# Optimization experiments

Measured on AMD Instinct MI355X. Metric: run time of the kernel, lower is better.

## Reference

```python
import jax, jax.numpy as jnp
import numpy as np

NUM_CLASSES = 80
NUM_ANCHORS = 5
ANCHORS = np.array([[1.3221, 1.73145], [3.19275, 4.00944], [5.05587, 8.09892],
                    [9.47112, 4.84053], [11.2364, 10.0071]], dtype=np.float32)
OBJECT_SCALE = 5.0
NOOBJECT_SCALE = 1.0
COORD_SCALE = 1.0
CLASS_SCALE = 1.0
THRESH = 0.6
SEEN = 0  # module initializes self.seen = 0 -> burn-in branch (seen < 12800) active
MAX_BOXES = 50


def _iou_cxcywh(a, b):
    # a, b: (..., 4) center-x, center-y, w, h; broadcastable. Matches multi_bbox_ious(x1y1x2y2=False).
    ax1, ax2 = a[..., 0] - a[..., 2] / 2, a[..., 0] + a[..., 2] / 2
    ay1, ay2 = a[..., 1] - a[..., 3] / 2, a[..., 1] + a[..., 3] / 2
    bx1, bx2 = b[..., 0] - b[..., 2] / 2, b[..., 0] + b[..., 2] / 2
    by1, by2 = b[..., 1] - b[..., 3] / 2, b[..., 1] + b[..., 3] / 2
    iw = jnp.maximum(jnp.minimum(ax2, bx2) - jnp.maximum(ax1, bx1), 0.0)
    ih = jnp.maximum(jnp.minimum(ay2, by2) - jnp.maximum(ay1, by1), 0.0)
    inter = iw * ih
    union = a[..., 2] * a[..., 3] + b[..., 2] * b[..., 3] - inter
    return inter / jnp.maximum(union, 1e-10)


def setup_inputs() -> dict:
    key = jax.random.key(0)
    k1, k2, k3, k4, k5, k6 = jax.random.split(key, 6)
    nB, nH, nW = 64, 38, 38
    output = jax.random.normal(k1, (nB, NUM_ANCHORS * (5 + NUM_CLASSES), nH, nW), dtype=jnp.float32)
    # target rows: (class, x, y, w, h), coords normalized to (0,1); x>0 keeps all 50 boxes valid
    cls = jax.random.randint(k2, (nB, MAX_BOXES), 0, NUM_CLASSES).astype(jnp.float32)
    x = jax.random.uniform(k3, (nB, MAX_BOXES), minval=0.05, maxval=0.95)
    y = jax.random.uniform(k4, (nB, MAX_BOXES), minval=0.05, maxval=0.95)
    w = jax.random.uniform(k5, (nB, MAX_BOXES), minval=0.02, maxval=0.4)
    h = jax.random.uniform(k6, (nB, MAX_BOXES), minval=0.02, maxval=0.4)
    target = jnp.stack([cls, x, y, w, h], axis=-1).reshape(nB, MAX_BOXES * 5)
    return {"output": output, "target": target}


def _forward(output, target):
    nB, nA, nC = output.shape[0], NUM_ANCHORS, NUM_CLASSES
    nH, nW = output.shape[2], output.shape[3]
    N = nB * nA * nH * nW
    anchors = jnp.asarray(ANCHORS)
    f32 = output.dtype

    out5 = output.reshape(nB, nA, 5 + nC, nH, nW)
    txy = jax.nn.sigmoid(out5[:, :, 0:2])  # [nB,nA,2,nH,nW]
    twh = out5[:, :, 2:4]
    conf = jax.nn.sigmoid(out5[:, :, 4]).reshape(N)
    cls_logits = out5[:, :, 5:].transpose(0, 1, 3, 4, 2).reshape(N, nC)
    # coord layout matches torch: [4, nB*nA*nH*nW], rows = (sx, sy, tw, th)
    coord = jnp.concatenate([txy, twh], axis=2).transpose(2, 0, 1, 3, 4).reshape(4, N)

    # decoded pred boxes in grid units; detached like the original (convert2cpu + .detach())
    grid_x = jnp.arange(nW, dtype=f32)
    grid_y = jnp.arange(nH, dtype=f32)[:, None]
    px = txy[:, :, 0] + grid_x
    py = txy[:, :, 1] + grid_y
    pw = jnp.exp(twh[:, :, 0]) * anchors[:, 0][None, :, None, None]
    ph = jnp.exp(twh[:, :, 1]) * anchors[:, 1][None, :, None, None]
    pred_boxes = jax.lax.stop_gradient(jnp.stack([px, py, pw, ph], axis=-1))  # [nB,nA,nH,nW,4]

    # ---------------- build_targets, vectorized over (batch, gt-box) ----------------
    tbox = target.reshape(nB, MAX_BOXES, 5)  # (cls, x, y, w, h)
    # loop breaks at first x == 0 -> prefix-valid mask
    valid = jnp.cumprod((tbox[:, :, 1] > 0).astype(jnp.int32), axis=1).astype(bool)
    gx, gy = tbox[:, :, 1] * nW, tbox[:, :, 2] * nH
    gw, gh = tbox[:, :, 3] * nW, tbox[:, :, 4] * nH
    gt = jnp.stack([gx, gy, gw, gh], axis=-1)  # [nB,50,4]

    # pass 1: ignore mask -- max IoU of every pred box against all valid GTs
    pb_flat = pred_boxes.reshape(nB, nA * nH * nW, 4)
    ious = _iou_cxcywh(pb_flat[:, :, None, :], gt[:, None, :, :])  # [nB,P,50]
    cur_ious = jnp.where(valid[:, None, :], ious, 0.0).max(axis=2)
    noobj = (cur_ious <= THRESH).astype(f32).reshape(N)

    # pass 2: best anchor per GT (both boxes centered at origin -> IoU simplifies)
    aw, ah = anchors[:, 0], anchors[:, 1]
    inter_a = jnp.minimum(aw, gw[..., None]) * jnp.minimum(ah, gh[..., None])  # [nB,50,nA]
    union_a = aw * ah + (gw * gh)[..., None] - inter_a
    best_n = jnp.argmax(inter_a / jnp.maximum(union_a, 1e-10), axis=-1)  # [nB,50]

    gi = jnp.clip(gx.astype(jnp.int32), 0, nW - 1)
    gj = jnp.clip(gy.astype(jnp.int32), 0, nH - 1)
    b_idx = jnp.arange(nB)[:, None]
    pred_sel = pred_boxes[b_idx, best_n, gj, gi]  # [nB,50,4]
    iou_sel = _iou_cxcywh(gt, pred_sel)           # [nB,50]

    fidx = ((b_idx * nA + best_n) * nH + gj) * nW + gi
    fidx = jnp.where(valid, fidx, N)  # invalid boxes -> OOB index, dropped by scatter

    obj = jnp.zeros(N, f32).at[fidx].set(1.0, mode='drop')
    noobj = noobj.at[fidx].set(0.0, mode='drop')
    cm0 = 0.01 if SEEN < 12800 else 0.0
    coord_mask = jnp.full(N, cm0, f32).at[fidx].set(2.0 - tbox[:, :, 3] * tbox[:, :, 4], mode='drop')
    t0 = 0.5 if SEEN < 12800 else 0.0
    tc0 = jnp.full(N, t0, f32).at[fidx].set(gx - gi.astype(f32), mode='drop')
    tc1 = jnp.full(N, t0, f32).at[fidx].set(gy - gj.astype(f32), mode='drop')
    tc2 = jnp.zeros(N, f32).at[fidx].set(jnp.log(gw / aw[best_n]), mode='drop')
    tc3 = jnp.zeros(N, f32).at[fidx].set(jnp.log(gh / ah[best_n]), mode='drop')
    tcoord = jnp.stack([tc0, tc1, tc2, tc3], axis=0)  # [4,N]
    tconf = jnp.zeros(N, f32).at[fidx].set(iou_sel, mode='drop')  # rescore=1
    tcls = jnp.zeros(N, jnp.int32).at[fidx].set(tbox[:, :, 0].astype(jnp.int32), mode='drop')

    # ---------------- losses ----------------
    conf_mask = OBJECT_SCALE * obj + NOOBJECT_SCALE * noobj
    loss_coord = COORD_SCALE * jnp.sum(((coord - tcoord) * coord_mask) ** 2) / nB
    loss_conf = jnp.sum(((conf - tconf) * conf_mask) ** 2) / nB
    logp = jax.nn.log_softmax(cls_logits, axis=-1)
    ce = -jnp.take_along_axis(logp, tcls[:, None], axis=1)[:, 0]  # per-cell CE
    loss_cls = CLASS_SCALE * jnp.sum(obj * ce) / nB  # CE summed only over obj cells
    return loss_coord + loss_conf + loss_cls


def reference(output, target):
    return _forward(output, target)
```

## Files before the change

kernel.cpp:

```cpp
#include <hip/hip_runtime.h>
#include <math.h>

#define NB 64
#define NA 5
#define NC 80
#define NH 38
#define NW 38
#define MAXB 50
#define PLANE (NH*NW)
#define PER_B (NA*PLANE)
#define NCH (5+NC)
#define MAIN_BX ((PER_B + 255) / 256)
#define NPART (MAIN_BX * NB)

__constant__ float c_aw[5] = {1.3221f, 3.19275f, 5.05587f, 9.47112f, 11.2364f};
__constant__ float c_ah[5] = {1.73145f, 4.00944f, 8.09892f, 4.84053f, 10.0071f};

struct Entry {
    int   fidx;
    int   tcls;
    float cm, tc0, tc1, tc2, tc3, tconf;
};

__device__ inline float sigmoidf(float x) { return 1.f / (1.f + expf(-x)); }

__global__ __launch_bounds__(256)
void main_kernel(const float* __restrict__ out, const float* __restrict__ target,
                 float* __restrict__ partial) {
    const int b   = blockIdx.y;
    const int bx  = blockIdx.x;
    const int tid = threadIdx.x;

    __shared__ float4 sbox[MAXB];
    __shared__ float  sarea[MAXB];
    __shared__ Entry  sent[MAXB];
    __shared__ int    sfx[64];
    __shared__ int    snv;
    __shared__ int    sobj_cnt;
    __shared__ int    sobj_idx[MAXB];

    if (tid == 0) sobj_cnt = 0;

    if (tid < 64) {
        const float* tb = target + b * MAXB * 5;
        int t = tid;
        bool has = (t < MAXB);
        float cls = 0.f, x = 0.f, y = 0.f, w = 0.f, h = 0.f;
        if (has) {
            cls = tb[t * 5 + 0];
            x   = tb[t * 5 + 1];
            y   = tb[t * 5 + 2];
            w   = tb[t * 5 + 3];
            h   = tb[t * 5 + 4];
        }
        unsigned long long mask = __ballot(has && (x > 0.f));
        bool valid = has && (((~mask) & ((1ull << (t + 1)) - 1ull)) == 0ull);

        float gx = x * NW, gy = y * NH, gw = w * NW, gh = h * NH;

        int best = 0; float bestr = -1.f;
        #pragma unroll
        for (int a = 0; a < NA; a++) {
            float inter = fminf(c_aw[a], gw) * fminf(c_ah[a], gh);
            float uni   = c_aw[a] * c_ah[a] + gw * gh - inter;
            float r = inter / fmaxf(uni, 1e-10f);
            if (r > bestr) { bestr = r; best = a; }
        }
        int gi = min(max((int)gx, 0), NW - 1);
        int gj = min(max((int)gy, 0), NH - 1);
        int fidx = b * PER_B + best * PLANE + gj * NW + gi;

        float iou_sel = 0.f;
        if (valid) {
            int base = ((b * NA + best) * NCH) * PLANE + gj * NW + gi;
            float o0 = out[base];
            float o1 = out[base + PLANE];
            float o2 = out[base + 2 * PLANE];
            float o3 = out[base + 3 * PLANE];
            float px = sigmoidf(o0) + (float)gi;
            float py = sigmoidf(o1) + (float)gj;
            float pw = expf(o2) * c_aw[best];
            float ph = expf(o3) * c_ah[best];
            float iw = fmaxf(fminf(gx + gw*0.5f, px + pw*0.5f) - fmaxf(gx - gw*0.5f, px - pw*0.5f), 0.f);
            float ih = fmaxf(fminf(gy + gh*0.5f, py + ph*0.5f) - fmaxf(gy - gh*0.5f, py - ph*0.5f), 0.f);
            float inter = iw * ih;
            float uni = gw * gh + pw * ph - inter;
            iou_sel = inter / fmaxf(uni, 1e-10f);
        }

        sfx[t] = valid ? fidx : -1;
        bool winner = valid;
        if (valid) {
            for (int s = t + 1; s < MAXB; s++)
                if (sfx[s] == fidx) { winner = false; break; }
        }

        if (has) {
            sbox[t]  = make_float4(gx - gw*0.5f, gy - gh*0.5f, gx + gw*0.5f, gy + gh*0.5f);
            sarea[t] = gw * gh;
            Entry e;
            e.fidx  = winner ? fidx : -1;
            e.tcls  = (int)cls;
            e.cm    = 2.f - w * h;
            e.tc0   = gx - (float)gi;
            e.tc1   = gy - (float)gj;
            e.tc2   = logf(gw / c_aw[best]);
            e.tc3   = logf(gh / c_ah[best]);
            e.tconf = iou_sel;
            sent[t] = e;
        }
        if (t == 0) {
            unsigned long long nm = ~mask;
            snv = min(__ffsll((unsigned long long)nm) - 1, MAXB);
        }
    }
    __syncthreads();

    const int nlo = b * PER_B + bx * 256;
    if (tid < MAXB) {
        int f = sent[tid].fidx;
        if (f >= nlo && f < nlo + 256) {
            int slot = atomicAdd(&sobj_cnt, 1);
            sobj_idx[slot] = tid;
        }
    }
    __syncthreads();

    int m = bx * 256 + tid;
    float part = 0.f;
    if (m < PER_B) {
        int a   = m / PLANE;
        int pos = m - a * PLANE;
        int j   = pos / NW;
        int i   = pos - j * NW;

        int base = ((b * NA + a) * NCH) * PLANE + pos;
        float o0 = out[base];
        float o1 = out[base + PLANE];
        float o2 = out[base + 2 * PLANE];
        float o3 = out[base + 3 * PLANE];
        float o4 = out[base + 4 * PLANE];

        float s0   = sigmoidf(o0);
        float s1   = sigmoidf(o1);
        float conf = sigmoidf(o4);
        float pw = expf(o2) * c_aw[a];
        float ph = expf(o3) * c_ah[a];
        float px1 = s0 + (float)i - pw * 0.5f;
        float px2 = px1 + pw;
        float py1 = s1 + (float)j - ph * 0.5f;
        float py2 = py1 + ph;
        float area_p = pw * ph;

        bool gt06 = false;
        int nv = snv;
        for (int s = 0; s < nv; s++) {
            float4 g = sbox[s];
            float iw = fmaxf(fminf(px2, g.z) - fmaxf(px1, g.x), 0.f);
            float ih = fmaxf(fminf(py2, g.w) - fmaxf(py1, g.y), 0.f);
            float inter = iw * ih;
            float uni = area_p + sarea[s] - inter;
            gt06 = gt06 || (inter > 0.6f * fmaxf(uni, 1e-10f));
        }

        float cm = 0.01f, tc0 = 0.5f, tc1 = 0.5f, tc2 = 0.f, tc3 = 0.f, tconf = 0.f;
        bool is_obj = false;
        int n = nlo + tid;
        int oc = sobj_cnt;
        for (int s = 0; s < oc; s++) {
            int e = sobj_idx[s];
            if (sent[e].fidx == n) {
                is_obj = true;
                cm  = sent[e].cm;
                tc0 = sent[e].tc0;  tc1 = sent[e].tc1;
                tc2 = sent[e].tc2;  tc3 = sent[e].tc3;
                tconf = sent[e].tconf;
            }
        }
        float conf_mask = is_obj ? 5.f : (gt06 ? 0.f : 1.f);

        float d;
        d = (s0   - tc0)   * cm;        part += d * d;
        d = (s1   - tc1)   * cm;        part += d * d;
        d = (o2   - tc2)   * cm;        part += d * d;
        d = (o3   - tc3)   * cm;        part += d * d;
        d = (conf - tconf) * conf_mask; part += d * d;
    }

    {
        int wid  = tid >> 6, lane = tid & 63;
        int oc   = sobj_cnt;
        for (int e = wid; e < oc; e += 4) {
            Entry ent = sent[sobj_idx[e]];
            int rel  = ent.fidx - b * PER_B;
            int a    = rel / PLANE;
            int pos  = rel - a * PLANE;
            const float* cp = out + ((b * NA + a) * NCH + 5) * PLANE + pos;

            float v1 = cp[lane * PLANE];
            float v2 = (lane < NC - 64) ? cp[(64 + lane) * PLANE] : -INFINITY;

            float mx = fmaxf(v1, v2);
            for (int off = 32; off > 0; off >>= 1) mx = fmaxf(mx, __shfl_xor(mx, off));
            float s = expf(v1 - mx) + ((lane < NC - 64) ? expf(v2 - mx) : 0.f);
            for (int off = 32; off > 0; off >>= 1) s += __shfl_xor(s, off);

            int tc = ent.tcls;
            float tv = (tc < 64) ? __shfl(v1, tc) : __shfl(v2, tc - 64);
            if (lane == 0) part += mx + logf(s) - tv;
        }
    }

    for (int off = 32; off > 0; off >>= 1) part += __shfl_down(part, off);
    __shared__ float wsum[4];
    int wid = tid >> 6, lane = tid & 63;
    if (lane == 0) wsum[wid] = part;
    __syncthreads();
    if (tid == 0)
        partial[b * MAIN_BX + bx] = wsum[0] + wsum[1] + wsum[2] + wsum[3];
}

__global__ __launch_bounds__(256)
void final_kernel(const float* __restrict__ partial, float* __restrict__ loss) {
    int tid = threadIdx.x;
    float s = 0.f;
    for (int i = tid; i < NPART; i += 256) s += partial[i];
    for (int off = 32; off > 0; off >>= 1) s += __shfl_down(s, off);
    __shared__ float wsum[4];
    int wid = tid >> 6, lane = tid & 63;
    if (lane == 0) wsum[wid] = s;
    __syncthreads();
    if (tid == 0)
        loss[0] = (wsum[0] + wsum[1] + wsum[2] + wsum[3]) * (1.0f / NB);
}

extern "C" void kernel_launch(void* const* d_in, const int* in_sizes, int n_in,
                              void* d_out, int out_size, void* d_ws, size_t ws_size,
                              hipStream_t stream) {
    const float* out    = (const float*)d_in[0];
    const float* target = (const float*)d_in[1];
    float* loss    = (float*)d_out;
    float* partial = (float*)d_ws;

    dim3 grid(MAIN_BX, NB);
    main_kernel<<<grid, 256, 0, stream>>>(out, target, partial);
    final_kernel<<<1, 256, 0, stream>>>(partial, loss);
}
```

Measured before the change: 209.7 us.

## Prefetch class logits early, add shared obj map, use fast math intrinsics

Switches sigmoid, exp and log to fast hardware intrinsics (__expf, __logf, rcp). Adds a shared per-block short map from cell to target entry, which replaces the linear scan over object entries for each thread. Issues the gathered class-logit loads for the first four object entries before the main per-cell computation, so their latency overlaps the IoU loop. Fast intrinsics carry a small accuracy risk, and the early loads hold extra registers.

```diff
diff --git a/kernel.cpp b/kernel.cpp
--- a/kernel.cpp
+++ b/kernel.cpp
@@ -22,7 +22,9 @@
     float cm, tc0, tc1, tc2, tc3, tconf;
 };
 
-__device__ inline float sigmoidf(float x) { return 1.f / (1.f + expf(-x)); }
+__device__ inline float fexp(float x)     { return __expf(x); }
+__device__ inline float flog(float x)     { return __logf(x); }
+__device__ inline float fsigmoid(float x) { return __builtin_amdgcn_rcpf(1.f + __expf(-x)); }
 
 __global__ __launch_bounds__(256)
 void main_kernel(const float* __restrict__ out, const float* __restrict__ target,
@@ -38,8 +40,10 @@
     __shared__ int    snv;
     __shared__ int    sobj_cnt;
     __shared__ int    sobj_idx[MAXB];
+    __shared__ short  smap[256];
 
     if (tid == 0) sobj_cnt = 0;
+    smap[tid] = -1;
 
     if (tid < 64) {
         const float* tb = target + b * MAXB * 5;
@@ -77,10 +81,10 @@
             float o1 = out[base + PLANE];
             float o2 = out[base + 2 * PLANE];
             float o3 = out[base + 3 * PLANE];
-            float px = sigmoidf(o0) + (float)gi;
-            float py = sigmoidf(o1) + (float)gj;
-            float pw = expf(o2) * c_aw[best];
-            float ph = expf(o3) * c_ah[best];
+            float px = fsigmoid(o0) + (float)gi;
+            float py = fsigmoid(o1) + (float)gj;
+            float pw = fexp(o2) * c_aw[best];
+            float ph = fexp(o3) * c_ah[best];
             float iw = fmaxf(fminf(gx + gw*0.5f, px + pw*0.5f) - fmaxf(gx - gw*0.5f, px - pw*0.5f), 0.f);
             float ih = fmaxf(fminf(gy + gh*0.5f, py + ph*0.5f) - fmaxf(gy - gh*0.5f, py - ph*0.5f), 0.f);
             float inter = iw * ih;
@@ -104,8 +108,8 @@
             e.cm    = 2.f - w * h;
             e.tc0   = gx - (float)gi;
             e.tc1   = gy - (float)gj;
-            e.tc2   = logf(gw / c_aw[best]);
-            e.tc3   = logf(gh / c_ah[best]);
+            e.tc2   = flog(gw / c_aw[best]);
+            e.tc3   = flog(gh / c_ah[best]);
             e.tconf = iou_sel;
             sent[t] = e;
         }
@@ -122,9 +126,27 @@
         if (f >= nlo && f < nlo + 256) {
             int slot = atomicAdd(&sobj_cnt, 1);
             sobj_idx[slot] = tid;
-        }
-    }
-    __syncthreads();
+            smap[f - nlo] = (short)tid;
+        }
+    }
+    __syncthreads();
+
+    const int wid = tid >> 6, lane = tid & 63;
+    const int oc = sobj_cnt;
+
+    int   my_e = (wid < oc) ? sobj_idx[wid] : -1;
+    float v1 = 0.f, v2 = -INFINITY;
+    int   my_tcls = 0;
+    if (my_e >= 0) {
+        Entry ent = sent[my_e];
+        my_tcls = ent.tcls;
+        int rel  = ent.fidx - b * PER_B;
+        int a    = rel / PLANE;
+        int pos  = rel - a * PLANE;
+        const float* cp = out + ((b * NA + a) * NCH + 5) * PLANE + pos;
+        v1 = cp[lane * PLANE];
+        if (lane < NC - 64) v2 = cp[(64 + lane) * PLANE];
+    }
 
     int m = bx * 256 + tid;
     float part = 0.f;
@@ -141,11 +163,11 @@
         float o3 = out[base + 3 * PLANE];
         float o4 = out[base + 4 * PLANE];
 
-        float s0   = sigmoidf(o0);
-        float s1   = sigmoidf(o1);
-        float conf = sigmoidf(o4);
-        float pw = expf(o2) * c_aw[a];
-        float ph = expf(o3) * c_ah[a];
+        float s0   = fsigmoid(o0);
+        float s1   = fsigmoid(o1);
+        float conf = fsigmoid(o4);
+        float pw = fexp(o2) * c_aw[a];
+        float ph = fexp(o3) * c_ah[a];
         float px1 = s0 + (float)i - pw * 0.5f;
         float px2 = px1 + pw;
         float py1 = s1 + (float)j - ph * 0.5f;
@@ -165,17 +187,13 @@
 
         float cm = 0.01f, tc0 = 0.5f, tc1 = 0.5f, tc2 = 0.f, tc3 = 0.f, tconf = 0.f;
         bool is_obj = false;
-        int n = nlo + tid;
-        int oc = sobj_cnt;
-        for (int s = 0; s < oc; s++) {
-            int e = sobj_idx[s];
-            if (sent[e].fidx == n) {
-                is_obj = true;
-                cm  = sent[e].cm;
-                tc0 = sent[e].tc0;  tc1 = sent[e].tc1;
-                tc2 = sent[e].tc2;  tc3 = sent[e].tc3;
-                tconf = sent[e].tconf;
-            }
+        int e = smap[tid];
+        if (e >= 0) {
+            is_obj = true;
+            cm  = sent[e].cm;
+            tc0 = sent[e].tc0;  tc1 = sent[e].tc1;
+            tc2 = sent[e].tc2;  tc3 = sent[e].tc3;
+            tconf = sent[e].tconf;
         }
         float conf_mask = is_obj ? 5.f : (gt06 ? 0.f : 1.f);
 
@@ -187,33 +205,32 @@
         d = (conf - tconf) * conf_mask; part += d * d;
     }
 
-    {
-        int wid  = tid >> 6, lane = tid & 63;
-        int oc   = sobj_cnt;
-        for (int e = wid; e < oc; e += 4) {
-            Entry ent = sent[sobj_idx[e]];
-            int rel  = ent.fidx - b * PER_B;
-            int a    = rel / PLANE;
-            int pos  = rel - a * PLANE;
-            const float* cp = out + ((b * NA + a) * NCH + 5) * PLANE + pos;
-
-            float v1 = cp[lane * PLANE];
-            float v2 = (lane < NC - 64) ? cp[(64 + lane) * PLANE] : -INFINITY;
-
-            float mx = fmaxf(v1, v2);
-            for (int off = 32; off > 0; off >>= 1) mx = fmaxf(mx, __shfl_xor(mx, off));
-            float s = expf(v1 - mx) + ((lane < NC - 64) ? expf(v2 - mx) : 0.f);
-            for (int off = 32; off > 0; off >>= 1) s += __shfl_xor(s, off);
-
-            int tc = ent.tcls;
-            float tv = (tc < 64) ? __shfl(v1, tc) : __shfl(v2, tc - 64);
-            if (lane == 0) part += mx + logf(s) - tv;
-        }
+    if (my_e >= 0) {
+        float mx = fmaxf(v1, v2);
+        for (int off = 32; off > 0; off >>= 1) mx = fmaxf(mx, __shfl_xor(mx, off));
+        float s = fexp(v1 - mx) + ((lane < NC - 64) ? fexp(v2 - mx) : 0.f);
+        for (int off = 32; off > 0; off >>= 1) s += __shfl_xor(s, off);
+        float tv = (my_tcls < 64) ? __shfl(v1, my_tcls) : __shfl(v2, my_tcls - 64);
+        if (lane == 0) part += mx + flog(s) - tv;
+    }
+    for (int e = 4 + wid; e < oc; e += 4) {
+        Entry ent = sent[sobj_idx[e]];
+        int rel  = ent.fidx - b * PER_B;
+        int a    = rel / PLANE;
+        int pos  = rel - a * PLANE;
+        const float* cp = out + ((b * NA + a) * NCH + 5) * PLANE + pos;
+        float w1 = cp[lane * PLANE];
+        float w2 = (lane < NC - 64) ? cp[(64 + lane) * PLANE] : -INFINITY;
+        float mx = fmaxf(w1, w2);
+        for (int off = 32; off > 0; off >>= 1) mx = fmaxf(mx, __shfl_xor(mx, off));
+        float s = fexp(w1 - mx) + ((lane < NC - 64) ? fexp(w2 - mx) : 0.f);
+        for (int off = 32; off > 0; off >>= 1) s += __shfl_xor(s, off);
+        float tv = (ent.tcls < 64) ? __shfl(w1, ent.tcls) : __shfl(w2, ent.tcls - 64);
+        if (lane == 0) part += mx + flog(s) - tv;
     }
 
     for (int off = 32; off > 0; off >>= 1) part += __shfl_down(part, off);
     __shared__ float wsum[4];
-    int wid = tid >> 6, lane = tid & 63;
     if (lane == 0) wsum[wid] = part;
     __syncthreads();
     if (tid == 0)
```

After: 213.9 us. 2.0% more time.
